# Kernel optimization log

Hardware: AMD Instinct MI355X
Metric: run time of the kernel (lower is better)

## Reference

```python
import jax, jax.numpy as jnp
import numpy as np

B, S, F_IN = 8, 4096, 256      # batch, frames, mel bins
C = 256                        # model_complexity (out_features of attention)
G = 8                          # n_heads (groups)
K = 31                         # w_size (local window, odd)
F_OUT = 88                     # output_features (piano keys)
PAD = (K - 1) // 2


def setup_inputs() -> dict:
    key = jax.random.key(0)
    ks = jax.random.split(key, 7)
    s = 0.05
    return {
        "spec": jax.random.normal(ks[0], (B, S, F_IN), jnp.float32),
        "W_q": jax.random.normal(ks[1], (F_IN, C), jnp.float32) * s,
        "W_k": jax.random.normal(ks[2], (F_IN, C), jnp.float32) * s,
        "W_v": jax.random.normal(ks[3], (F_IN, C), jnp.float32) * s,
        "rel": jax.random.normal(ks[4], (C, K), jnp.float32),
        "W_lin": jax.random.normal(ks[5], (C, F_OUT), jnp.float32) * s,
        "b_lin": jax.random.normal(ks[6], (F_OUT,), jnp.float32) * s,
    }


def reference(spec, W_q, W_k, W_v, rel, W_lin, b_lin):
    b, s, _ = spec.shape
    d = C // G  # per-head dim
    # QKV projections (no bias, as in the module)
    q = spec @ W_q                                             # [B,S,C]
    padded = jnp.pad(spec, ((0, 0), (PAD, PAD), (0, 0)))       # [B,S+2p,F]
    k = padded @ W_k                                           # [B,S+2p,C]
    v = padded @ W_v
    # unfold: window index [S,K]
    idx = jnp.arange(s)[:, None] + jnp.arange(K)[None, :]      # [S,K]
    kw = jnp.transpose(k[:, idx, :], (0, 1, 3, 2))             # [B,S,C,K]
    vw = jnp.transpose(v[:, idx, :], (0, 1, 3, 2))             # [B,S,C,K]
    kw = kw + rel                                              # positional bias [C,K]
    kw = kw.reshape(b, s, G, d, K)
    vw = vw.reshape(b, s, G, d, K)
    qh = q.reshape(b, s, G, d)
    energy = jnp.einsum('bsgd,bsgdk->bsgk', qh, kw)            # [B,S,G,K]
    attn = jax.nn.softmax(energy, axis=-1)                     # [B,S,G,K]
    out = jnp.einsum('bsgk,bsgdk->bsgd', attn, vw).reshape(b, s, C)
    frame_pred = jax.nn.sigmoid(out @ W_lin + b_lin)           # [B,S,F_OUT]
    return frame_pred, attn
```

## Files before the change

kernel.cpp:

```cpp
#include <hip/hip_runtime.h>
#include <hip/hip_bf16.h>
#include <math.h>

#define B_   8
#define S_   4096
#define FIN  256
#define C_   256
#define G_   8
#define D_   32
#define K_   31
#define PAD_ 15
#define FOUT 88

typedef __bf16 bf16;
typedef __attribute__((ext_vector_type(8))) __bf16 bf16x8;
typedef __attribute__((ext_vector_type(4))) __bf16 bf16x4;
typedef __attribute__((ext_vector_type(4))) float f32x4;

#define MFMA16(A, B, C) __builtin_amdgcn_mfma_f32_16x16x32_bf16(A, B, C, 0, 0, 0)

__global__ __launch_bounds__(256) void split_spec(
    const float* __restrict__ spec, bf16* __restrict__ sh, bf16* __restrict__ sl)
{
    const size_t base = ((size_t)blockIdx.x * 256 + threadIdx.x) * 8;
    float4 x0 = *(const float4*)&spec[base];
    float4 x1 = *(const float4*)&spec[base + 4];
    float xs[8] = {x0.x, x0.y, x0.z, x0.w, x1.x, x1.y, x1.z, x1.w};
    bf16x8 H, L;
#pragma unroll
    for (int j = 0; j < 8; ++j) {
        bf16 h = (bf16)xs[j];
        H[j] = h;
        L[j] = (bf16)(xs[j] - (float)h);
    }
    *(bf16x8*)&sh[base] = H;
    *(bf16x8*)&sl[base] = L;
}

__global__ void split_w(const float* __restrict__ Wq, const float* __restrict__ Wk,
                        const float* __restrict__ Wv,
                        bf16* __restrict__ bth, bf16* __restrict__ btl)
{
    const int k = blockIdx.x;
    const int w = blockIdx.y;
    const int n = threadIdx.x;
    const float* W = (w == 0) ? Wq : (w == 1) ? Wk : Wv;
    float x = W[(size_t)k * 256 + n];
    bf16 h = (bf16)x;
    bf16 l = (bf16)(x - (float)h);
    size_t o = (size_t)w * 65536 + (size_t)n * 256 + k;
    bth[o] = h;
    btl[o] = l;
}

__global__ void split_wl(const float* __restrict__ Wl,
                         bf16* __restrict__ wlh, bf16* __restrict__ wll)
{
    const int k = blockIdx.x;
    const int n = threadIdx.x;
    const float x = (n < FOUT) ? Wl[(size_t)k * FOUT + n] : 0.f;
    bf16 h = (bf16)x;
    bf16 l = (bf16)(x - (float)h);
    wlh[(size_t)n * 256 + k] = h;
    wll[(size_t)n * 256 + k] = l;
}

__global__ void vt_pad(bf16* __restrict__ Vt) {
    const int idx = blockIdx.x * 256 + threadIdx.x;
    const int bd  = idx >> 4;
    const int pos = (idx & 15) * 4;
    const int off = (pos < 16) ? pos : 4096 + pos;
    bf16x4 z = {};
    *(bf16x4*)&Vt[(size_t)bd * 4160 + off] = z;
}

__global__ void rel_prep(const float* __restrict__ rel, char* __restrict__ relsG) {
    const int idx = blockIdx.x * 256 + threadIdx.x;
    const int g = idx >> 10, k = (idx >> 5) & 31, d = idx & 31;
    const float v = (k < 31) ? rel[(size_t)(g * 32 + d) * 31 + k] : 0.f;
    bf16 h = (bf16)v;
    bf16 l = (bf16)(v - (float)h);
    const int bo = g * 2048 + k * 64 + (((d >> 3) ^ (k & 3)) << 4) + (d & 7) * 2;
    *(bf16*)(relsG + bo)         = h;
    *(bf16*)(relsG + 16384 + bo) = l;
}

__device__ __forceinline__ void gload16(const bf16* g, bf16* l) {
    __builtin_amdgcn_global_load_lds(
        (const __attribute__((address_space(1))) void*)g,
        (__attribute__((address_space(3))) void*)l, 16, 0, 0);
}

__device__ __forceinline__ void stage_tile(const bf16* g, bf16* l, int t) {
    const int lg = ((t & 3) ^ ((t >> 3) & 3)) * 8;
    const int r0 = t >> 2;
    const int r1 = 64 + (t >> 2);
    const int u0 = (t & ~63) * 8;
    gload16(g + (size_t)r0 * 256 + lg, l + u0);
    gload16(g + (size_t)r1 * 256 + lg, l + u0 + 2048);
}

__device__ __forceinline__ bf16x8 frag_ld(const bf16* l, int r, int cl) {
    return *(const bf16x8*)&l[r * 32 + ((cl ^ ((r >> 1) & 3)) << 3)];
}

__global__ __launch_bounds__(256) void qkv_mfma(
    const bf16* __restrict__ sh, const bf16* __restrict__ sl,
    const bf16* __restrict__ bth, const bf16* __restrict__ btl,
    bf16* __restrict__ Qh, bf16* __restrict__ Ql,
    bf16* __restrict__ Kh, bf16* __restrict__ Kl,
    bf16* __restrict__ Vt)
{
    __shared__ bf16 lds[4 * 4096];

    const int t   = threadIdx.x;
    const int swz = ((blockIdx.x & 7) * 192) + (blockIdx.x >> 3);
    const int mt  = swz / 6, nt = swz % 6;
    const int wt  = nt >> 1;
    const int m0  = mt * 128, n0 = (nt & 1) * 128;
    const bool three = (wt < 2);

    const bf16* ah_g = sh  + (size_t)m0 * 256;
    const bf16* al_g = sl  + (size_t)m0 * 256;
    const bf16* bh_g = bth + (size_t)wt * 65536 + (size_t)n0 * 256;
    const bf16* bl_g = btl + (size_t)wt * 65536 + (size_t)n0 * 256;

    const int lane = t & 63, wid = t >> 6;
    const int wr = (wid >> 1) * 64, wc = (wid & 1) * 64;
    const int fr = lane & 15, cl = lane >> 4;

    f32x4 acc[4][4];
#pragma unroll
    for (int m = 0; m < 4; ++m)
#pragma unroll
        for (int n = 0; n < 4; ++n)
            acc[m][n] = (f32x4){0.f, 0.f, 0.f, 0.f};

    for (int ks = 0; ks < 8; ++ks) {
        const int ko = ks * 32;
        stage_tile(ah_g + ko, lds, t);
        if (three) stage_tile(al_g + ko, lds + 4096, t);
        stage_tile(bh_g + ko, lds + 8192, t);
        stage_tile(bl_g + ko, lds + 12288, t);
        __syncthreads();

        bf16x8 ah[4], bh[4], bl[4];
#pragma unroll
        for (int m = 0; m < 4; ++m) ah[m] = frag_ld(lds, wr + m * 16 + fr, cl);
#pragma unroll
        for (int n = 0; n < 4; ++n) {
            bh[n] = frag_ld(lds + 8192,  wc + n * 16 + fr, cl);
            bl[n] = frag_ld(lds + 12288, wc + n * 16 + fr, cl);
        }
#pragma unroll
        for (int m = 0; m < 4; ++m)
#pragma unroll
            for (int n = 0; n < 4; ++n) {
                acc[m][n] = MFMA16(ah[m], bh[n], acc[m][n]);
                acc[m][n] = MFMA16(ah[m], bl[n], acc[m][n]);
            }
        if (three) {
            bf16x8 al[4];
#pragma unroll
            for (int m = 0; m < 4; ++m) al[m] = frag_ld(lds + 4096, wr + m * 16 + fr, cl);
#pragma unroll
            for (int m = 0; m < 4; ++m)
#pragma unroll
                for (int n = 0; n < 4; ++n)
                    acc[m][n] = MFMA16(al[m], bh[n], acc[m][n]);
        }
        __syncthreads();
    }

    if (wt < 2) {
        bf16* Oh = (wt == 0) ? Qh : Kh;
        bf16* Ol = (wt == 0) ? Ql : Kl;
#pragma unroll
        for (int m = 0; m < 4; ++m) {
            const int gr = m0 + wr + m * 16 + cl * 4;
#pragma unroll
            for (int n = 0; n < 4; ++n) {
                const int gc = n0 + wc + n * 16 + fr;
#pragma unroll
                for (int i = 0; i < 4; ++i) {
                    const float v = acc[m][n][i];
                    const bf16 hh = (bf16)v;
                    const size_t off = (size_t)(gr + i) * 256 + gc;
                    Oh[off] = hh;
                    Ol[off] = (bf16)(v - (float)hh);
                }
            }
        }
    } else {
#pragma unroll
        for (int m = 0; m < 4; ++m) {
            const int gr = m0 + wr + m * 16 + cl * 4;
            const int bb = gr >> 12, sr = gr & 4095;
#pragma unroll
            for (int n = 0; n < 4; ++n) {
                const int gc = n0 + wc + n * 16 + fr;
                bf16x4 pk;
#pragma unroll
                for (int i = 0; i < 4; ++i) pk[i] = (bf16)acc[m][n][i];
                *(bf16x4*)&Vt[(size_t)(bb * 256 + gc) * 4160 + 16 + sr] = pk;
            }
        }
    }
}

__global__ __launch_bounds__(256) void attn_mfma(
    const bf16* __restrict__ Qh, const bf16* __restrict__ Ql,
    const bf16* __restrict__ Kh, const bf16* __restrict__ Kl,
    const bf16* __restrict__ Vt, const char* __restrict__ relsG,
    float* __restrict__ attn, bf16* __restrict__ Obf)
{
    __shared__ char ldsb[51200];
    const int t = threadIdx.x;

#pragma unroll
    for (int j = 0; j < 8; ++j) {
        const int off = (j * 256 + t) * 16;
        *(uint4*)(ldsb + off) = *(const uint4*)(relsG + off);
    }
    __syncthreads();

    const int wid  = t >> 6;
    const int lane = t & 63;
    const int fr   = lane & 15;
    const int q    = lane >> 4;
    const int f7   = fr & 7;

    const int bid2 = ((blockIdx.x & 7) << 8) | (blockIdx.x >> 3);
    const int sg0  = bid2 << 4;
    const int b    = sg0 >> 12;
    const int s0   = sg0 & 4095;

    float* Rbuf = (float*)(ldsb + 32768 + wid * 2304);
    bf16*  Pbuf = (bf16*) (ldsb + 41984 + wid * 2304);

    {
        uint* p32 = (uint*)Pbuf;
#pragma unroll
        for (int j = 0; j < 9; ++j) p32[lane + 64 * j] = 0u;
    }

    const size_t rowQ = (size_t)(sg0 + fr) * 256;

#pragma unroll
    for (int h = 0; h < 2; ++h) {
        const int g   = wid * 2 + h;
        const int dof = g * 32 + q * 8;

        const bf16x8 qh8 = *(const bf16x8*)&Qh[rowQ + dof];
        const bf16x8 ql8 = *(const bf16x8*)&Ql[rowQ + dof];

        f32x4 e0, e1, e2;
#pragma unroll
        for (int tau = 0; tau < 3; ++tau) {
            const int trel = s0 - 16 + tau * 16 + fr;
            bf16x8 kh8 = {}, kl8 = {};
            if ((unsigned)trel < 4096u) {
                const size_t rk = ((size_t)(b << 12) + trel) * 256 + dof;
                kh8 = *(const bf16x8*)&Kh[rk];
                kl8 = *(const bf16x8*)&Kl[rk];
            }
            f32x4 a = (f32x4){0.f, 0.f, 0.f, 0.f};
            a = MFMA16(kh8, qh8, a);
            a = MFMA16(kh8, ql8, a);
            a = MFMA16(kl8, qh8, a);
            if (tau == 0) e0 = a; else if (tau == 1) e1 = a; else e2 = a;
        }

#pragma unroll
        for (int kap = 0; kap < 2; ++kap) {
            const int krow = kap * 16 + fr;
            const int bo = (g << 11) + krow * 64 + ((q ^ (krow & 3)) << 4);
            const bf16x8 rh8 = *(const bf16x8*)(ldsb + bo);
            const bf16x8 rl8 = *(const bf16x8*)(ldsb + 16384 + bo);
            f32x4 rc = (f32x4){0.f, 0.f, 0.f, 0.f};
            rc = MFMA16(rh8, qh8, rc);
            rc = MFMA16(rh8, ql8, rc);
            rc = MFMA16(rl8, qh8, rc);
#pragma unroll
            for (int r = 0; r < 4; ++r)
                Rbuf[(kap * 16 + q * 4 + r) * 18 + fr] = rc[r];
        }

        float ev[3][4];
        float mx = -3.0e38f;
#pragma unroll
        for (int tau = 0; tau < 3; ++tau) {
#pragma unroll
            for (int r = 0; r < 4; ++r) {
                const int rp = q * 4 + r;
                const int kk = tau * 16 + rp - fr - 1;
                const float eb = (tau == 0) ? e0[r] : (tau == 1) ? e1[r] : e2[r];
                float v = eb + Rbuf[(kk & 31) * 18 + fr];
                const bool valid = (tau == 1) || ((tau == 0) ? (rp > fr) : (rp < fr));
                v = valid ? v : -3.0e38f;
                ev[tau][r] = v;
                mx = fmaxf(mx, v);
            }
        }
        mx = fmaxf(mx, __shfl_xor(mx, 16));
        mx = fmaxf(mx, __shfl_xor(mx, 32));
        float sum = 0.f;
#pragma unroll
        for (int tau = 0; tau < 3; ++tau)
#pragma unroll
            for (int r = 0; r < 4; ++r) {
                const float p = __expf(ev[tau][r] - mx);
                ev[tau][r] = p;
                sum += p;
            }
        sum += __shfl_xor(sum, 16);
        sum += __shfl_xor(sum, 32);
        const float inv = 1.f / sum;

        float* arow = &attn[((size_t)(sg0 + fr) * 8 + g) * 31];
#pragma unroll
        for (int tau = 0; tau < 3; ++tau)
#pragma unroll
            for (int r = 0; r < 4; ++r) {
                const int rp = q * 4 + r;
                const int kk = tau * 16 + rp - fr - 1;
                const bool valid = (tau == 1) || ((tau == 0) ? (rp > fr) : (rp < fr));
                if (valid) {
                    const float p = ev[tau][r] * inv;
                    arow[kk] = p;
                    const int tl = tau * 16 + rp;
                    Pbuf[fr * 72 + (((tl >> 3) ^ f7) << 3) + (tl & 7)] = (bf16)p;
                }
            }

        const bf16x8 a0 = *(const bf16x8*)&Pbuf[fr * 72 + ((q ^ f7) << 3)];
        const bf16x8 a1 = *(const bf16x8*)&Pbuf[fr * 72 + (((4 + q) ^ f7) << 3)];
#pragma unroll
        for (int dl = 0; dl < 2; ++dl) {
            const size_t vrow = (size_t)(b * 256 + g * 32 + dl * 16 + fr) * 4160
                              + s0 + q * 8;
            const bf16x8 v0 = *(const bf16x8*)&Vt[vrow];
            const bf16x8 v1 = *(const bf16x8*)&Vt[vrow + 32];
            f32x4 o = (f32x4){0.f, 0.f, 0.f, 0.f};
            o = MFMA16(a0, v0, o);
            o = MFMA16(a1, v1, o);
#pragma unroll
            for (int r = 0; r < 4; ++r)
                Obf[(size_t)(sg0 + q * 4 + r) * 256 + g * 32 + dl * 16 + fr] = (bf16)o[r];
        }
    }
}

__global__ __launch_bounds__(256) void frame_mfma(
    const bf16* __restrict__ O,
    const bf16* __restrict__ wlh, const bf16* __restrict__ wll,
    const float* __restrict__ bl, float* __restrict__ frame)
{
    __shared__ bf16 lds[3 * 4096];

    const int t  = threadIdx.x;
    const int m0 = blockIdx.x * 128;

    const bf16* a_g = O + (size_t)m0 * 256;

    const int lane = t & 63, wid = t >> 6;
    const int wr = (wid >> 1) * 64, wc = (wid & 1) * 64;
    const int fr = lane & 15, cl = lane >> 4;

    f32x4 acc[4][4];
#pragma unroll
    for (int m = 0; m < 4; ++m)
#pragma unroll
        for (int n = 0; n < 4; ++n)
            acc[m][n] = (f32x4){0.f, 0.f, 0.f, 0.f};

    for (int ks = 0; ks < 8; ++ks) {
        const int ko = ks * 32;
        stage_tile(a_g + ko, lds, t);
        stage_tile(wlh + ko, lds + 4096, t);
        stage_tile(wll + ko, lds + 8192, t);
        __syncthreads();

        bf16x8 ah[4], bh[4], bl4[4];
#pragma unroll
        for (int m = 0; m < 4; ++m) ah[m] = frag_ld(lds, wr + m * 16 + fr, cl);
#pragma unroll
        for (int n = 0; n < 4; ++n) {
            bh[n]  = frag_ld(lds + 4096, wc + n * 16 + fr, cl);
            bl4[n] = frag_ld(lds + 8192, wc + n * 16 + fr, cl);
        }
#pragma unroll
        for (int m = 0; m < 4; ++m)
#pragma unroll
            for (int n = 0; n < 4; ++n) {
                acc[m][n] = MFMA16(ah[m], bh[n],  acc[m][n]);
                acc[m][n] = MFMA16(ah[m], bl4[n], acc[m][n]);
            }
        __syncthreads();
    }

#pragma unroll
    for (int m = 0; m < 4; ++m) {
        const int gr = m0 + wr + m * 16 + cl * 4;
#pragma unroll
        for (int n = 0; n < 4; ++n) {
            const int gc = wc + n * 16 + fr;
            if (gc < FOUT) {
                const float bb = bl[gc];
#pragma unroll
                for (int i = 0; i < 4; ++i) {
                    const float x = acc[m][n][i] + bb;
                    frame[(size_t)(gr + i) * FOUT + gc] = 1.f / (1.f + __expf(-x));
                }
            }
        }
    }
}

extern "C" void kernel_launch(void* const* d_in, const int* in_sizes, int n_in,
                              void* d_out, int out_size, void* d_ws, size_t ws_size,
                              hipStream_t stream) {
    (void)in_sizes; (void)n_in; (void)out_size; (void)ws_size;
    const float* spec = (const float*)d_in[0];
    const float* Wq   = (const float*)d_in[1];
    const float* Wk   = (const float*)d_in[2];
    const float* Wv   = (const float*)d_in[3];
    const float* rel  = (const float*)d_in[4];
    const float* Wl   = (const float*)d_in[5];
    const float* bl   = (const float*)d_in[6];

    float* frame = (float*)d_out;
    float* attn  = frame + (size_t)B_ * S_ * FOUT;

    bf16* sh    = (bf16*)d_out;
    bf16* sl    = sh + (size_t)B_ * S_ * FIN;
    bf16* bth   = (bf16*)((char*)d_out + 33554432);
    bf16* btl   = bth + 3 * 65536;
    char* relsG = (char*)d_out;

    bf16* Qh  = (bf16*)d_ws;
    bf16* Ql  = Qh + (size_t)8388608;
    bf16* Kh  = Ql + (size_t)8388608;
    bf16* Kl  = Kh + (size_t)8388608;
    bf16* Vt  = Kl + (size_t)8388608;
    bf16* wlh = Vt + (size_t)8 * 256 * 4160;
    bf16* wll = wlh + 128 * 256;

    vt_pad    <<<dim3(128),     256, 0, stream>>>(Vt);
    split_spec<<<dim3(4096),    256, 0, stream>>>(spec, sh, sl);
    split_w   <<<dim3(256, 3),  256, 0, stream>>>(Wq, Wk, Wv, bth, btl);
    split_wl  <<<dim3(256),     128, 0, stream>>>(Wl, wlh, wll);
    qkv_mfma  <<<dim3(1536),    256, 0, stream>>>(sh, sl, bth, btl, Qh, Ql, Kh, Kl, Vt);
    rel_prep  <<<dim3(32),      256, 0, stream>>>(rel, relsG);
    attn_mfma <<<dim3(2048),    256, 0, stream>>>(Qh, Ql, Kh, Kl, Vt, relsG, attn, Qh);
    frame_mfma<<<dim3(256),     256, 0, stream>>>(Qh, wlh, wll, bl, frame);
}
```

Baseline: 129.2 us.

## Double-buffer QKV GEMM tiles and restage attention stores through LDS

The QKV GEMM now double-buffers its LDS tiles and prefetches the next K-slice before computing the current one, which drops the per-iteration barrier wait on loads. The attention kernel no longer copies the rel table into LDS; it reads rel fragments straight from global (L2) memory and shrinks LDS use, which should allow more resident blocks. Attention probabilities are staged through LDS so the attn output is written with coalesced row stores. The P·V MFMA operands are swapped so the output is written as packed 4-element vectors. There is a risk: the second loop iteration prefetches into the buffer that other waves may still be reading, because there is no barrier at the end of the loop (one syncthreads remains after compute in the loop body, not shown). The diff also adds more global loads for rel.

Result: no change. 128.5 us (-0.5%).

```diff
diff --git a/kernel.cpp b/kernel.cpp
--- a/kernel.cpp
+++ b/kernel.cpp
@@ -74,15 +74,14 @@
     *(bf16x4*)&Vt[(size_t)bd * 4160 + off] = z;
 }
 
-__global__ void rel_prep(const float* __restrict__ rel, char* __restrict__ relsG) {
+__global__ void rel_prep(const float* __restrict__ rel,
+                         bf16* __restrict__ relH, bf16* __restrict__ relL) {
     const int idx = blockIdx.x * 256 + threadIdx.x;
     const int g = idx >> 10, k = (idx >> 5) & 31, d = idx & 31;
     const float v = (k < 31) ? rel[(size_t)(g * 32 + d) * 31 + k] : 0.f;
     bf16 h = (bf16)v;
-    bf16 l = (bf16)(v - (float)h);
-    const int bo = g * 2048 + k * 64 + (((d >> 3) ^ (k & 3)) << 4) + (d & 7) * 2;
-    *(bf16*)(relsG + bo)         = h;
-    *(bf16*)(relsG + 16384 + bo) = l;
+    relH[idx] = h;
+    relL[idx] = (bf16)(v - (float)h);
 }
 
 __device__ __forceinline__ void gload16(const bf16* g, bf16* l) {
@@ -111,7 +110,7 @@
     bf16* __restrict__ Kh, bf16* __restrict__ Kl,
     bf16* __restrict__ Vt)
 {
-    __shared__ bf16 lds[4 * 4096];
+    __shared__ bf16 lds[2 * 4 * 4096];
 
     const int t   = threadIdx.x;
     const int swz = ((blockIdx.x & 7) * 192) + (blockIdx.x >> 3);
@@ -136,21 +135,30 @@
         for (int n = 0; n < 4; ++n)
             acc[m][n] = (f32x4){0.f, 0.f, 0.f, 0.f};
 
+    stage_tile(ah_g, lds, t);
+    if (three) stage_tile(al_g, lds + 4096, t);
+    stage_tile(bh_g, lds + 8192, t);
+    stage_tile(bl_g, lds + 12288, t);
+    __syncthreads();
+
     for (int ks = 0; ks < 8; ++ks) {
-        const int ko = ks * 32;
-        stage_tile(ah_g + ko, lds, t);
-        if (three) stage_tile(al_g + ko, lds + 4096, t);
-        stage_tile(bh_g + ko, lds + 8192, t);
-        stage_tile(bl_g + ko, lds + 12288, t);
-        __syncthreads();
+        const int cur = (ks & 1) * 16384;
+        if (ks < 7) {
+            const int nxt = 16384 - cur;
+            const int ko  = (ks + 1) * 32;
+            stage_tile(ah_g + ko, lds + nxt, t);
+            if (three) stage_tile(al_g + ko, lds + nxt + 4096, t);
+            stage_tile(bh_g + ko, lds + nxt + 8192, t);
+            stage_tile(bl_g + ko, lds + nxt + 12288, t);
+        }
 
         bf16x8 ah[4], bh[4], bl[4];
 #pragma unroll
-        for (int m = 0; m < 4; ++m) ah[m] = frag_ld(lds, wr + m * 16 + fr, cl);
+        for (int m = 0; m < 4; ++m) ah[m] = frag_ld(lds + cur, wr + m * 16 + fr, cl);
 #pragma unroll
         for (int n = 0; n < 4; ++n) {
-            bh[n] = frag_ld(lds + 8192,  wc + n * 16 + fr, cl);
-            bl[n] = frag_ld(lds + 12288, wc + n * 16 + fr, cl);
+            bh[n] = frag_ld(lds + cur + 8192,  wc + n * 16 + fr, cl);
+            bl[n] = frag_ld(lds + cur + 12288, wc + n * 16 + fr, cl);
         }
 #pragma unroll
         for (int m = 0; m < 4; ++m)
@@ -162,7 +170,7 @@
         if (three) {
             bf16x8 al[4];
 #pragma unroll
-            for (int m = 0; m < 4; ++m) al[m] = frag_ld(lds + 4096, wr + m * 16 + fr, cl);
+            for (int m = 0; m < 4; ++m) al[m] = frag_ld(lds + cur + 4096, wr + m * 16 + fr, cl);
 #pragma unroll
             for (int m = 0; m < 4; ++m)
 #pragma unroll
@@ -211,32 +219,29 @@
 __global__ __launch_bounds__(256) void attn_mfma(
     const bf16* __restrict__ Qh, const bf16* __restrict__ Ql,
     const bf16* __restrict__ Kh, const bf16* __restrict__ Kl,
-    const bf16* __restrict__ Vt, const char* __restrict__ relsG,
+    const bf16* __restrict__ Vt,
+    const bf16* __restrict__ relH, const bf16* __restrict__ relL,
     float* __restrict__ attn, bf16* __restrict__ Obf)
 {
-    __shared__ char ldsb[51200];
-    const int t = threadIdx.x;
-
-#pragma unroll
-    for (int j = 0; j < 8; ++j) {
-        const int off = (j * 256 + t) * 16;
-        *(uint4*)(ldsb + off) = *(const uint4*)(relsG + off);
-    }
-    __syncthreads();
-
+    __shared__ char ldsb[18432];
+
+    const int t    = threadIdx.x;
     const int wid  = t >> 6;
     const int lane = t & 63;
     const int fr   = lane & 15;
     const int q    = lane >> 4;
     const int f7   = fr & 7;
+    const int sl   = lane >> 2;
+    const int jj   = lane & 3;
 
     const int bid2 = ((blockIdx.x & 7) << 8) | (blockIdx.x >> 3);
     const int sg0  = bid2 << 4;
     const int b    = sg0 >> 12;
     const int s0   = sg0 & 4095;
 
-    float* Rbuf = (float*)(ldsb + 32768 + wid * 2304);
-    bf16*  Pbuf = (bf16*) (ldsb + 41984 + wid * 2304);
+    float* Rbuf = (float*)(ldsb + wid * 4608);
+    float* Pf32 = Rbuf;
+    bf16*  Pbuf = (bf16*) (ldsb + wid * 4608 + 2304);
 
     {
         uint* p32 = (uint*)Pbuf;
@@ -248,6 +253,7 @@
 
 #pragma unroll
     for (int h = 0; h < 2; ++h) {
+        asm volatile("" ::: "memory");
         const int g   = wid * 2 + h;
         const int dof = g * 32 + q * 8;
 
@@ -273,10 +279,9 @@
 
 #pragma unroll
         for (int kap = 0; kap < 2; ++kap) {
-            const int krow = kap * 16 + fr;
-            const int bo = (g << 11) + krow * 64 + ((q ^ (krow & 3)) << 4);
-            const bf16x8 rh8 = *(const bf16x8*)(ldsb + bo);
-            const bf16x8 rl8 = *(const bf16x8*)(ldsb + 16384 + bo);
+            const size_t ro = (size_t)(g * 32 + kap * 16 + fr) * 32 + q * 8;
+            const bf16x8 rh8 = *(const bf16x8*)&relH[ro];
+            const bf16x8 rl8 = *(const bf16x8*)&relL[ro];
             f32x4 rc = (f32x4){0.f, 0.f, 0.f, 0.f};
             rc = MFMA16(rh8, qh8, rc);
             rc = MFMA16(rh8, ql8, rc);
@@ -317,7 +322,6 @@
         sum += __shfl_xor(sum, 32);
         const float inv = 1.f / sum;
 
-        float* arow = &attn[((size_t)(sg0 + fr) * 8 + g) * 31];
 #pragma unroll
         for (int tau = 0; tau < 3; ++tau)
 #pragma unroll
@@ -327,12 +331,23 @@
                 const bool valid = (tau == 1) || ((tau == 0) ? (rp > fr) : (rp < fr));
                 if (valid) {
                     const float p = ev[tau][r] * inv;
-                    arow[kk] = p;
+                    Pf32[fr * 36 + kk] = p;
                     const int tl = tau * 16 + rp;
                     Pbuf[fr * 72 + (((tl >> 3) ^ f7) << 3) + (tl & 7)] = (bf16)p;
                 }
             }
 
+        asm volatile("" ::: "memory");
+        {
+            float* arow = &attn[((size_t)(sg0 + sl) * 8 + g) * 31];
+#pragma unroll
+            for (int i = 0; i < 8; ++i) {
+                const int k = jj + 4 * i;
+                if (k < 31) arow[k] = Pf32[sl * 36 + k];
+            }
+        }
+
+        asm volatile("" ::: "memory");
         const bf16x8 a0 = *(const bf16x8*)&Pbuf[fr * 72 + ((q ^ f7) << 3)];
         const bf16x8 a1 = *(const bf16x8*)&Pbuf[fr * 72 + (((4 + q) ^ f7) << 3)];
 #pragma unroll
@@ -342,11 +357,12 @@
             const bf16x8 v0 = *(const bf16x8*)&Vt[vrow];
             const bf16x8 v1 = *(const bf16x8*)&Vt[vrow + 32];
             f32x4 o = (f32x4){0.f, 0.f, 0.f, 0.f};
-            o = MFMA16(a0, v0, o);
-            o = MFMA16(a1, v1, o);
-#pragma unroll
-            for (int r = 0; r < 4; ++r)
-                Obf[(size_t)(sg0 + q * 4 + r) * 256 + g * 32 + dl * 16 + fr] = (bf16)o[r];
+            o = MFMA16(v0, a0, o);
+            o = MFMA16(v1, a1, o);
+            bf16x4 pk;
+#pragma unroll
+            for (int r = 0; r < 4; ++r) pk[r] = (bf16)o[r];
+            *(bf16x4*)&Obf[(size_t)(sg0 + fr) * 256 + g * 32 + dl * 16 + (q << 2)] = pk;
         }
     }
 }
@@ -432,11 +448,12 @@
     float* frame = (float*)d_out;
     float* attn  = frame + (size_t)B_ * S_ * FOUT;
 
-    bf16* sh    = (bf16*)d_out;
-    bf16* sl    = sh + (size_t)B_ * S_ * FIN;
-    bf16* bth   = (bf16*)((char*)d_out + 33554432);
-    bf16* btl   = bth + 3 * 65536;
-    char* relsG = (char*)d_out;
+    bf16* sh   = (bf16*)d_out;
+    bf16* sl   = sh + (size_t)B_ * S_ * FIN;
+    bf16* bth  = (bf16*)((char*)d_out + 33554432);
+    bf16* btl  = bth + 3 * 65536;
+    bf16* relH = (bf16*)d_out;
+    bf16* relL = relH + 8192;
 
     bf16* Qh  = (bf16*)d_ws;
     bf16* Ql  = Qh + (size_t)8388608;
@@ -451,7 +468,7 @@
     split_w   <<<dim3(256, 3),  256, 0, stream>>>(Wq, Wk, Wv, bth, btl);
     split_wl  <<<dim3(256),     128, 0, stream>>>(Wl, wlh, wll);
     qkv_mfma  <<<dim3(1536),    256, 0, stream>>>(sh, sl, bth, btl, Qh, Ql, Kh, Kl, Vt);
-    rel_prep  <<<dim3(32),      256, 0, stream>>>(rel, relsG);
-    attn_mfma <<<dim3(2048),    256, 0, stream>>>(Qh, Ql, Kh, Kl, Vt, relsG, attn, Qh);
+    rel_prep  <<<dim3(32),      256, 0, stream>>>(rel, relH, relL);
+    attn_mfma <<<dim3(2048),    256, 0, stream>>>(Qh, Ql, Kh, Kl, Vt, relH, relL, attn, Qh);
     frame_mfma<<<dim3(256),     256, 0, stream>>>(Qh, wlh, wll, bl, frame);
 }
```
